# Optimization experiments

Measured on AMD Instinct MI355X. Metric: run time of the kernel, lower is better.

Reference implementation:

```python
import jax, jax.numpy as jnp
import numpy as np

NUM_SEQS = 16
NUM_HEADS = 32
NUM_KV_HEADS = 8
HEAD_SIZE = 128
BLOCK_SIZE = 16
X = 8  # vectorized key-cache packing factor
MAX_CTX = 4096
MAX_BLOCKS = MAX_CTX // BLOCK_SIZE
NUM_BLOCKS = NUM_SEQS * MAX_BLOCKS
SCALE = 0.08838834764831845  # 1/sqrt(128)
NEG_INF = -1e30


def setup_inputs() -> dict:
    key0 = jax.random.key(0)
    ks = jax.random.split(key0, 5)
    query = jax.random.normal(ks[0], (NUM_SEQS, 1, NUM_HEADS * HEAD_SIZE), jnp.float32)
    key = jax.random.normal(ks[1], (NUM_SEQS, 1, NUM_KV_HEADS * HEAD_SIZE), jnp.float32)
    value = jax.random.normal(ks[2], (NUM_SEQS, 1, NUM_KV_HEADS * HEAD_SIZE), jnp.float32)
    key_cache = jax.random.normal(ks[3], (NUM_BLOCKS, NUM_KV_HEADS, HEAD_SIZE // X, BLOCK_SIZE, X), jnp.float32)
    value_cache = jax.random.normal(ks[4], (NUM_BLOCKS, NUM_KV_HEADS, HEAD_SIZE, BLOCK_SIZE), jnp.float32)
    rng = np.random.default_rng(0)
    block_tables = rng.permutation(NUM_BLOCKS).reshape(NUM_SEQS, MAX_BLOCKS).astype(np.int32)
    context_lens = rng.integers(256, MAX_CTX + 1, size=(NUM_SEQS,)).astype(np.int32)
    last = context_lens - 1
    slots = block_tables[np.arange(NUM_SEQS), last // BLOCK_SIZE].astype(np.int64) * BLOCK_SIZE + (last % BLOCK_SIZE)
    slot_mapping = slots.reshape(NUM_SEQS, 1)
    return {
        'query': query, 'key': key, 'value': value,
        'key_cache': key_cache, 'value_cache': value_cache,
        'block_tables': jnp.asarray(block_tables),
        'context_lens': jnp.asarray(context_lens),
        'slot_mapping': jnp.asarray(slot_mapping),
    }


def _paged_attention_decode(query, key, value, key_cache, value_cache, block_tables, context_lens, slot_mapping):
    S, L1, hidden = query.shape  # L1 == 1 (decode)
    nb, kvH, _, bs, x = key_cache.shape
    D = value_cache.shape[2]
    H = hidden // D
    G = H // kvH  # queries per kv head
    maxB = block_tables.shape[1]

    q = query.reshape(S, H, D)
    k_new = key.reshape(S, kvH, D)
    v_new = value.reshape(S, kvH, D)

    # --- reshape_and_cache: write new K/V into paged caches ---
    sm = slot_mapping.reshape(-1)
    blk, off = sm // bs, sm % bs
    key_cache = key_cache.at[blk, :, :, off, :].set(k_new.reshape(S, kvH, D // x, x))
    value_cache = value_cache.at[blk, :, :, off].set(v_new)

    # --- gather paged KV via block tables ---
    # key_cache [nb,kvH,D/x,bs,x] -> [nb,kvH,bs,D]
    kc = key_cache.transpose(0, 1, 3, 2, 4).reshape(nb, kvH, bs, D)
    vc = value_cache.transpose(0, 1, 3, 2)  # [nb,kvH,bs,D]
    keys = kc[block_tables].transpose(0, 1, 3, 2, 4).reshape(S, maxB * bs, kvH, D)
    vals = vc[block_tables].transpose(0, 1, 3, 2, 4).reshape(S, maxB * bs, kvH, D)

    # --- GQA attention with context-length masking ---
    qg = q.reshape(S, kvH, G, D)
    scores = jnp.einsum('skgd,slkd->skgl', qg, keys) * jnp.asarray(SCALE, q.dtype)
    valid = jnp.arange(maxB * bs)[None, :] < context_lens[:, None]  # [S,L]
    scores = jnp.where(valid[:, None, None, :], scores, NEG_INF)
    probs = jax.nn.softmax(scores, axis=-1)
    out = jnp.einsum('skgl,slkd->skgd', probs, vals)
    return out.reshape(S, 1, H * D)


def reference(query, key, value, key_cache, value_cache, block_tables, context_lens, slot_mapping):
    return _paged_attention_decode(query, key, value, key_cache, value_cache,
                                   block_tables, context_lens, slot_mapping)
```

## Files before the change

### kernel.cpp

```cpp
#include <hip/hip_runtime.h>

#define NSEQ   16
#define KVH    8
#define NG     4
#define HD     128
#define BS     16
#define MAXB   256
#define PART   256
#define NPART  16
#define PSTRIDE 520
#define SCALE_F 0.08838834764831845f

__global__ __launch_bounds__(256) void pa_partial_kernel(
    const float* __restrict__ query,
    const float* __restrict__ key,
    const float* __restrict__ value,
    const float* __restrict__ key_cache,
    const float* __restrict__ value_cache,
    const int*   __restrict__ block_tables,
    const int*   __restrict__ context_lens,
    float*       __restrict__ ws)
{
    const int bid = blockIdx.x;
    const int p   = bid & (NPART - 1);
    const int kvh = (bid >> 4) & (KVH - 1);
    const int s   = bid >> 7;

    const int ctx = context_lens[s];
    const int t0  = p * PART;
    if (t0 >= ctx) return;

    __shared__ float p_lds[NG * PART];
    __shared__ float o_lds[NG * HD];
    __shared__ float red[20];

    const int tid = threadIdx.x;
    const float* q = query + (size_t)s * (KVH * NG * HD) + (size_t)kvh * (NG * HD);

    const int t    = t0 + tid;
    const int bt   = block_tables[s * MAXB + (t >> 4)];
    const int off  = t & 15;
    const float* kb = key_cache + (size_t)bt * (KVH * HD * BS)
                                + (size_t)kvh * (HD * BS) + off * 8;

    float sc[NG] = {0.f, 0.f, 0.f, 0.f};
    #pragma unroll
    for (int j = 0; j < 16; ++j) {
        const float4 ka = *(const float4*)(kb + j * 128);
        const float4 kc = *(const float4*)(kb + j * 128 + 4);
        #pragma unroll
        for (int g = 0; g < NG; ++g) {
            sc[g] += q[g * HD + j * 8 + 0] * ka.x + q[g * HD + j * 8 + 1] * ka.y
                   + q[g * HD + j * 8 + 2] * ka.z + q[g * HD + j * 8 + 3] * ka.w
                   + q[g * HD + j * 8 + 4] * kc.x + q[g * HD + j * 8 + 5] * kc.y
                   + q[g * HD + j * 8 + 6] * kc.z + q[g * HD + j * 8 + 7] * kc.w;
        }
    }

    if (t == ctx - 1) {
        const float4* kn4 = (const float4*)(key + ((size_t)s * KVH + kvh) * HD);
        float ns[NG] = {0.f, 0.f, 0.f, 0.f};
        #pragma unroll
        for (int c = 0; c < 32; ++c) {
            const float4 k4 = kn4[c];
            #pragma unroll
            for (int g = 0; g < NG; ++g) {
                ns[g] += q[g * HD + c * 4 + 0] * k4.x + q[g * HD + c * 4 + 1] * k4.y
                       + q[g * HD + c * 4 + 2] * k4.z + q[g * HD + c * 4 + 3] * k4.w;
            }
        }
        #pragma unroll
        for (int g = 0; g < NG; ++g) sc[g] = ns[g];
    }

    float mval;
    if (t < ctx) {
        #pragma unroll
        for (int g = 0; g < NG; ++g) sc[g] *= SCALE_F;
        mval = fmaxf(fmaxf(sc[0], sc[1]), fmaxf(sc[2], sc[3]));
    } else {
        #pragma unroll
        for (int g = 0; g < NG; ++g) sc[g] = -1e30f;
        mval = -1e30f;
    }

    #pragma unroll
    for (int o = 32; o; o >>= 1) mval = fmaxf(mval, __shfl_xor(mval, o));
    const int wave = tid >> 6;
    if ((tid & 63) == 0) red[wave] = mval;
    __syncthreads();
    const float m = fmaxf(fmaxf(red[0], red[1]), fmaxf(red[2], red[3]));

    const float p0 = __expf(sc[0] - m);
    const float p1 = __expf(sc[1] - m);
    const float p2 = __expf(sc[2] - m);
    const float p3 = __expf(sc[3] - m);
    p_lds[0 * PART + tid] = p0;
    p_lds[1 * PART + tid] = p1;
    p_lds[2 * PART + tid] = p2;
    p_lds[3 * PART + tid] = p3;

    float l0 = p0, l1 = p1, l2 = p2, l3 = p3;
    #pragma unroll
    for (int o = 32; o; o >>= 1) {
        l0 += __shfl_xor(l0, o);
        l1 += __shfl_xor(l1, o);
        l2 += __shfl_xor(l2, o);
        l3 += __shfl_xor(l3, o);
    }
    if ((tid & 63) == 0) {
        red[4 + wave * 4 + 0] = l0;
        red[4 + wave * 4 + 1] = l1;
        red[4 + wave * 4 + 2] = l2;
        red[4 + wave * 4 + 3] = l3;
    }
    __syncthreads();

    const int d = tid & 127;
    const int h = tid >> 7;

    int btv[8];
    #pragma unroll
    for (int b = 0; b < 8; ++b)
        btv[b] = block_tables[s * MAXB + (t0 >> 4) + h * 8 + b];

    float a0 = 0.f, a1 = 0.f, a2 = 0.f, a3 = 0.f;
    const float4* pl4 = (const float4*)p_lds;
    #pragma unroll 2
    for (int b = 0; b < 8; ++b) {
        const int tb = h * 8 + b;
        const float* vb = value_cache + (size_t)btv[b] * (KVH * HD * BS)
                                      + (size_t)kvh * (HD * BS) + d * BS;
        #pragma unroll
        for (int c = 0; c < 4; ++c) {
            const float4 v4  = *(const float4*)(vb + c * 4);
            const float4 pg0 = pl4[0 * 64 + tb * 4 + c];
            const float4 pg1 = pl4[1 * 64 + tb * 4 + c];
            const float4 pg2 = pl4[2 * 64 + tb * 4 + c];
            const float4 pg3 = pl4[3 * 64 + tb * 4 + c];
            a0 += pg0.x*v4.x + pg0.y*v4.y + pg0.z*v4.z + pg0.w*v4.w;
            a1 += pg1.x*v4.x + pg1.y*v4.y + pg1.z*v4.z + pg1.w*v4.w;
            a2 += pg2.x*v4.x + pg2.y*v4.y + pg2.z*v4.z + pg2.w*v4.w;
            a3 += pg3.x*v4.x + pg3.y*v4.y + pg3.z*v4.z + pg3.w*v4.w;
        }
    }

    const int tlnew = ctx - 1 - t0;
    if (tlnew >= h * 128 && tlnew < h * 128 + 128) {
        const int btn = block_tables[s * MAXB + ((ctx - 1) >> 4)];
        const float vold = value_cache[(size_t)btn * (KVH * HD * BS)
                                       + (size_t)kvh * (HD * BS) + d * BS + ((ctx - 1) & 15)];
        const float vnew = value[((size_t)s * KVH + kvh) * HD + d];
        const float dv = vnew - vold;
        a0 += p_lds[0 * PART + tlnew] * dv;
        a1 += p_lds[1 * PART + tlnew] * dv;
        a2 += p_lds[2 * PART + tlnew] * dv;
        a3 += p_lds[3 * PART + tlnew] * dv;
    }

    if (h == 1) {
        o_lds[0 * HD + d] = a0;
        o_lds[1 * HD + d] = a1;
        o_lds[2 * HD + d] = a2;
        o_lds[3 * HD + d] = a3;
    }
    __syncthreads();

    float* rec = ws + (size_t)bid * PSTRIDE;
    if (h == 0) {
        a0 += o_lds[0 * HD + d];
        a1 += o_lds[1 * HD + d];
        a2 += o_lds[2 * HD + d];
        a3 += o_lds[3 * HD + d];
        rec[0 * HD + d] = a0;
        rec[1 * HD + d] = a1;
        rec[2 * HD + d] = a2;
        rec[3 * HD + d] = a3;
    }
    if (tid < 4) {
        rec[512 + tid] = red[4 + tid] + red[8 + tid] + red[12 + tid] + red[16 + tid];
    }
    if (tid == 4) rec[516] = m;
}

__global__ __launch_bounds__(128) void pa_reduce_kernel(
    const float* __restrict__ ws,
    const int*   __restrict__ context_lens,
    float*       __restrict__ out)
{
    const int b    = blockIdx.x;
    const int g    = b & 3;
    const int pair = b >> 2;
    const int s    = pair >> 3;
    const int kvh  = pair & 7;
    const int ctx  = context_lens[s];
    const int np   = (ctx + PART - 1) / PART;

    const int d = threadIdx.x;
    const float* base = ws + (size_t)pair * NPART * PSTRIDE;

    float M = -1e30f;
    for (int p2 = 0; p2 < np; ++p2) M = fmaxf(M, base[p2 * PSTRIDE + 516]);

    float L = 0.f, acc = 0.f;
    for (int p2 = 0; p2 < np; ++p2) {
        const float* rec = base + p2 * PSTRIDE;
        const float w = __expf(rec[516] - M);
        L   += w * rec[512 + g];
        acc += w * rec[g * HD + d];
    }

    out[(size_t)s * (KVH * NG * HD) + (size_t)(kvh * NG + g) * HD + d] = acc / L;
}

extern "C" void kernel_launch(void* const* d_in, const int* in_sizes, int n_in,
                              void* d_out, int out_size, void* d_ws, size_t ws_size,
                              hipStream_t stream) {
    const float* query       = (const float*)d_in[0];
    const float* key         = (const float*)d_in[1];
    const float* value       = (const float*)d_in[2];
    const float* key_cache   = (const float*)d_in[3];
    const float* value_cache = (const float*)d_in[4];
    const int*   block_tables  = (const int*)d_in[5];
    const int*   context_lens  = (const int*)d_in[6];

    float* out = (float*)d_out;
    float* ws  = (float*)d_ws;

    pa_partial_kernel<<<NSEQ * KVH * NPART, 256, 0, stream>>>(
        query, key, value, key_cache, value_cache, block_tables, context_lens, ws);
    pa_reduce_kernel<<<NSEQ * KVH * NG, 128, 0, stream>>>(ws, context_lens, out);
}
```

Baseline: 90.23 us.

## Make each wave compute an independent 64-token softmax partial and merge at end

Each of the four waves now handles its own 64-token slice end to end: it computes scores, a wave-local max and sum, and the PV product for that slice. The waves then merge their results with one rescaled combine after a single barrier. This removes two block-wide barriers and lets waves run ahead independently. Waves whose slice lies past the context length skip the K and V loads entirely. In exchange it uses more LDS for per-wave output buffers, adds extra exp and rescale work, and each wave now loops over both halves of the head dimension.

```diff
diff --git a/kernel.cpp b/kernel.cpp
--- a/kernel.cpp
+++ b/kernel.cpp
@@ -8,6 +8,7 @@
 #define MAXB   256
 #define PART   256
 #define NPART  16
+#define WPT    64
 #define PSTRIDE 520
 #define SCALE_F 0.08838834764831845f
 
@@ -30,157 +31,157 @@
     const int t0  = p * PART;
     if (t0 >= ctx) return;
 
-    __shared__ float p_lds[NG * PART];
-    __shared__ float o_lds[NG * HD];
-    __shared__ float red[20];
-
-    const int tid = threadIdx.x;
+    __shared__ float p_lds[4][NG][WPT];
+    __shared__ float o_lds[4][NG * HD];
+    __shared__ float ml_lds[4][8];
+
+    const int tid  = threadIdx.x;
+    const int wv   = tid >> 6;
+    const int lane = tid & 63;
+    const int tw0  = t0 + wv * WPT;
+    const bool wact = (tw0 < ctx);
+
     const float* q = query + (size_t)s * (KVH * NG * HD) + (size_t)kvh * (NG * HD);
 
-    const int t    = t0 + tid;
-    const int bt   = block_tables[s * MAXB + (t >> 4)];
-    const int off  = t & 15;
-    const float* kb = key_cache + (size_t)bt * (KVH * HD * BS)
-                                + (size_t)kvh * (HD * BS) + off * 8;
-
-    float sc[NG] = {0.f, 0.f, 0.f, 0.f};
+    float m_w = -1e30f;
+    float l_w[NG] = {0.f, 0.f, 0.f, 0.f};
+
+    if (wact) {
+        const int t  = tw0 + lane;
+        const int bt = block_tables[s * MAXB + (t >> 4)];
+        const float* kb = key_cache + (size_t)bt * (KVH * HD * BS)
+                                    + (size_t)kvh * (HD * BS) + (t & 15) * 8;
+
+        float sc[NG] = {0.f, 0.f, 0.f, 0.f};
+        #pragma unroll
+        for (int j = 0; j < 16; ++j) {
+            const float4 ka = *(const float4*)(kb + j * 128);
+            const float4 kc = *(const float4*)(kb + j * 128 + 4);
+            #pragma unroll
+            for (int g = 0; g < NG; ++g) {
+                sc[g] += q[g * HD + j * 8 + 0] * ka.x + q[g * HD + j * 8 + 1] * ka.y
+                       + q[g * HD + j * 8 + 2] * ka.z + q[g * HD + j * 8 + 3] * ka.w
+                       + q[g * HD + j * 8 + 4] * kc.x + q[g * HD + j * 8 + 5] * kc.y
+                       + q[g * HD + j * 8 + 6] * kc.z + q[g * HD + j * 8 + 7] * kc.w;
+            }
+        }
+
+        if (t == ctx - 1) {
+            const float4* kn4 = (const float4*)(key + ((size_t)s * KVH + kvh) * HD);
+            float ns[NG] = {0.f, 0.f, 0.f, 0.f};
+            #pragma unroll
+            for (int c = 0; c < 32; ++c) {
+                const float4 k4 = kn4[c];
+                #pragma unroll
+                for (int g = 0; g < NG; ++g) {
+                    ns[g] += q[g * HD + c * 4 + 0] * k4.x + q[g * HD + c * 4 + 1] * k4.y
+                           + q[g * HD + c * 4 + 2] * k4.z + q[g * HD + c * 4 + 3] * k4.w;
+                }
+            }
+            #pragma unroll
+            for (int g = 0; g < NG; ++g) sc[g] = ns[g];
+        }
+
+        float mv;
+        if (t < ctx) {
+            #pragma unroll
+            for (int g = 0; g < NG; ++g) sc[g] *= SCALE_F;
+            mv = fmaxf(fmaxf(sc[0], sc[1]), fmaxf(sc[2], sc[3]));
+        } else {
+            #pragma unroll
+            for (int g = 0; g < NG; ++g) sc[g] = -1e30f;
+            mv = -1e30f;
+        }
+
+        #pragma unroll
+        for (int o = 32; o; o >>= 1) mv = fmaxf(mv, __shfl_xor(mv, o));
+        m_w = mv;
+
+        float pr[NG];
+        #pragma unroll
+        for (int g = 0; g < NG; ++g) {
+            pr[g] = __expf(sc[g] - m_w);
+            p_lds[wv][g][lane] = pr[g];
+            l_w[g] = pr[g];
+        }
+        #pragma unroll
+        for (int o = 32; o; o >>= 1) {
+            l_w[0] += __shfl_xor(l_w[0], o);
+            l_w[1] += __shfl_xor(l_w[1], o);
+            l_w[2] += __shfl_xor(l_w[2], o);
+            l_w[3] += __shfl_xor(l_w[3], o);
+        }
+    }
+
+    if (lane == 0) {
+        ml_lds[wv][0] = m_w;
+        #pragma unroll
+        for (int g = 0; g < NG; ++g) ml_lds[wv][1 + g] = l_w[g];
+    }
+
+    if (wact) {
+        const int nbv = min(4, (ctx - tw0 + 15) >> 4);
+        int btv[4];
+        #pragma unroll
+        for (int b = 0; b < 4; ++b)
+            btv[b] = block_tables[s * MAXB + (tw0 >> 4) + b];
+
+        const int tl = ctx - 1 - tw0;
+        const float4* pl4 = (const float4*)&p_lds[wv][0][0];
+
+        #pragma unroll 2
+        for (int half = 0; half < 2; ++half) {
+            const int d = lane + half * 64;
+            float a[NG] = {0.f, 0.f, 0.f, 0.f};
+            for (int b = 0; b < nbv; ++b) {
+                const float* vb = value_cache + (size_t)btv[b] * (KVH * HD * BS)
+                                              + (size_t)kvh * (HD * BS) + d * BS;
+                #pragma unroll
+                for (int c = 0; c < 4; ++c) {
+                    const float4 v4 = *(const float4*)(vb + c * 4);
+                    #pragma unroll
+                    for (int g = 0; g < NG; ++g) {
+                        const float4 pg = pl4[g * 16 + b * 4 + c];
+                        a[g] += pg.x * v4.x + pg.y * v4.y + pg.z * v4.z + pg.w * v4.w;
+                    }
+                }
+            }
+            if (tl >= 0 && tl < WPT) {
+                const int btn = block_tables[s * MAXB + ((ctx - 1) >> 4)];
+                const float vold = value_cache[(size_t)btn * (KVH * HD * BS)
+                                               + (size_t)kvh * (HD * BS) + d * BS + ((ctx - 1) & 15)];
+                const float vnew = value[((size_t)s * KVH + kvh) * HD + d];
+                const float dv = vnew - vold;
+                #pragma unroll
+                for (int g = 0; g < NG; ++g) a[g] += p_lds[wv][g][tl] * dv;
+            }
+            #pragma unroll
+            for (int g = 0; g < NG; ++g) o_lds[wv][g * HD + d] = a[g];
+        }
+    } else {
+        #pragma unroll
+        for (int i = 0; i < 8; ++i) o_lds[wv][i * 64 + lane] = 0.f;
+    }
+
+    __syncthreads();
+
+    const float m0 = ml_lds[0][0], m1 = ml_lds[1][0], m2 = ml_lds[2][0], m3 = ml_lds[3][0];
+    const float M  = fmaxf(fmaxf(m0, m1), fmaxf(m2, m3));
+    const float w0 = __expf(m0 - M), w1 = __expf(m1 - M);
+    const float w2 = __expf(m2 - M), w3 = __expf(m3 - M);
+
+    float* rec = ws + (size_t)bid * PSTRIDE;
     #pragma unroll
-    for (int j = 0; j < 16; ++j) {
-        const float4 ka = *(const float4*)(kb + j * 128);
-        const float4 kc = *(const float4*)(kb + j * 128 + 4);
-        #pragma unroll
-        for (int g = 0; g < NG; ++g) {
-            sc[g] += q[g * HD + j * 8 + 0] * ka.x + q[g * HD + j * 8 + 1] * ka.y
-                   + q[g * HD + j * 8 + 2] * ka.z + q[g * HD + j * 8 + 3] * ka.w
-                   + q[g * HD + j * 8 + 4] * kc.x + q[g * HD + j * 8 + 5] * kc.y
-                   + q[g * HD + j * 8 + 6] * kc.z + q[g * HD + j * 8 + 7] * kc.w;
-        }
-    }
-
-    if (t == ctx - 1) {
-        const float4* kn4 = (const float4*)(key + ((size_t)s * KVH + kvh) * HD);
-        float ns[NG] = {0.f, 0.f, 0.f, 0.f};
-        #pragma unroll
-        for (int c = 0; c < 32; ++c) {
-            const float4 k4 = kn4[c];
-            #pragma unroll
-            for (int g = 0; g < NG; ++g) {
-                ns[g] += q[g * HD + c * 4 + 0] * k4.x + q[g * HD + c * 4 + 1] * k4.y
-                       + q[g * HD + c * 4 + 2] * k4.z + q[g * HD + c * 4 + 3] * k4.w;
-            }
-        }
-        #pragma unroll
-        for (int g = 0; g < NG; ++g) sc[g] = ns[g];
-    }
-
-    float mval;
-    if (t < ctx) {
-        #pragma unroll
-        for (int g = 0; g < NG; ++g) sc[g] *= SCALE_F;
-        mval = fmaxf(fmaxf(sc[0], sc[1]), fmaxf(sc[2], sc[3]));
-    } else {
-        #pragma unroll
-        for (int g = 0; g < NG; ++g) sc[g] = -1e30f;
-        mval = -1e30f;
-    }
-
-    #pragma unroll
-    for (int o = 32; o; o >>= 1) mval = fmaxf(mval, __shfl_xor(mval, o));
-    const int wave = tid >> 6;
-    if ((tid & 63) == 0) red[wave] = mval;
-    __syncthreads();
-    const float m = fmaxf(fmaxf(red[0], red[1]), fmaxf(red[2], red[3]));
-
-    const float p0 = __expf(sc[0] - m);
-    const float p1 = __expf(sc[1] - m);
-    const float p2 = __expf(sc[2] - m);
-    const float p3 = __expf(sc[3] - m);
-    p_lds[0 * PART + tid] = p0;
-    p_lds[1 * PART + tid] = p1;
-    p_lds[2 * PART + tid] = p2;
-    p_lds[3 * PART + tid] = p3;
-
-    float l0 = p0, l1 = p1, l2 = p2, l3 = p3;
-    #pragma unroll
-    for (int o = 32; o; o >>= 1) {
-        l0 += __shfl_xor(l0, o);
-        l1 += __shfl_xor(l1, o);
-        l2 += __shfl_xor(l2, o);
-        l3 += __shfl_xor(l3, o);
-    }
-    if ((tid & 63) == 0) {
-        red[4 + wave * 4 + 0] = l0;
-        red[4 + wave * 4 + 1] = l1;
-        red[4 + wave * 4 + 2] = l2;
-        red[4 + wave * 4 + 3] = l3;
-    }
-    __syncthreads();
-
-    const int d = tid & 127;
-    const int h = tid >> 7;
-
-    int btv[8];
-    #pragma unroll
-    for (int b = 0; b < 8; ++b)
-        btv[b] = block_tables[s * MAXB + (t0 >> 4) + h * 8 + b];
-
-    float a0 = 0.f, a1 = 0.f, a2 = 0.f, a3 = 0.f;
-    const float4* pl4 = (const float4*)p_lds;
-    #pragma unroll 2
-    for (int b = 0; b < 8; ++b) {
-        const int tb = h * 8 + b;
-        const float* vb = value_cache + (size_t)btv[b] * (KVH * HD * BS)
-                                      + (size_t)kvh * (HD * BS) + d * BS;
-        #pragma unroll
-        for (int c = 0; c < 4; ++c) {
-            const float4 v4  = *(const float4*)(vb + c * 4);
-            const float4 pg0 = pl4[0 * 64 + tb * 4 + c];
-            const float4 pg1 = pl4[1 * 64 + tb * 4 + c];
-            const float4 pg2 = pl4[2 * 64 + tb * 4 + c];
-            const float4 pg3 = pl4[3 * 64 + tb * 4 + c];
-            a0 += pg0.x*v4.x + pg0.y*v4.y + pg0.z*v4.z + pg0.w*v4.w;
-            a1 += pg1.x*v4.x + pg1.y*v4.y + pg1.z*v4.z + pg1.w*v4.w;
-            a2 += pg2.x*v4.x + pg2.y*v4.y + pg2.z*v4.z + pg2.w*v4.w;
-            a3 += pg3.x*v4.x + pg3.y*v4.y + pg3.z*v4.z + pg3.w*v4.w;
-        }
-    }
-
-    const int tlnew = ctx - 1 - t0;
-    if (tlnew >= h * 128 && tlnew < h * 128 + 128) {
-        const int btn = block_tables[s * MAXB + ((ctx - 1) >> 4)];
-        const float vold = value_cache[(size_t)btn * (KVH * HD * BS)
-                                       + (size_t)kvh * (HD * BS) + d * BS + ((ctx - 1) & 15)];
-        const float vnew = value[((size_t)s * KVH + kvh) * HD + d];
-        const float dv = vnew - vold;
-        a0 += p_lds[0 * PART + tlnew] * dv;
-        a1 += p_lds[1 * PART + tlnew] * dv;
-        a2 += p_lds[2 * PART + tlnew] * dv;
-        a3 += p_lds[3 * PART + tlnew] * dv;
-    }
-
-    if (h == 1) {
-        o_lds[0 * HD + d] = a0;
-        o_lds[1 * HD + d] = a1;
-        o_lds[2 * HD + d] = a2;
-        o_lds[3 * HD + d] = a3;
-    }
-    __syncthreads();
-
-    float* rec = ws + (size_t)bid * PSTRIDE;
-    if (h == 0) {
-        a0 += o_lds[0 * HD + d];
-        a1 += o_lds[1 * HD + d];
-        a2 += o_lds[2 * HD + d];
-        a3 += o_lds[3 * HD + d];
-        rec[0 * HD + d] = a0;
-        rec[1 * HD + d] = a1;
-        rec[2 * HD + d] = a2;
-        rec[3 * HD + d] = a3;
-    }
-    if (tid < 4) {
-        rec[512 + tid] = red[4 + tid] + red[8 + tid] + red[12 + tid] + red[16 + tid];
-    }
-    if (tid == 4) rec[516] = m;
+    for (int r = 0; r < 2; ++r) {
+        const int idx = tid + r * 256;
+        rec[idx] = w0 * o_lds[0][idx] + w1 * o_lds[1][idx]
+                 + w2 * o_lds[2][idx] + w3 * o_lds[3][idx];
+    }
+    if (tid < NG) {
+        rec[512 + tid] = w0 * ml_lds[0][1 + tid] + w1 * ml_lds[1][1 + tid]
+                       + w2 * ml_lds[2][1 + tid] + w3 * ml_lds[3][1 + tid];
+    }
+    if (tid == 4) rec[516] = M;
 }
 
 __global__ __launch_bounds__(128) void pa_reduce_kernel(
```

Measured after the change: 85.93 us. 1.05x faster.
